# Optimization experiments

Measured on AMD Instinct MI355X. Metric: run time of the kernel, lower is better.

## Reference

```python
import jax, jax.numpy as jnp
import numpy as np

N = 200000   # nodes
R = 4        # relations
E = 1000000  # edges per relation
B = 1024     # graphs in batch


def _graph_conv(h, s, d, ew, W, b):
    """DGL GraphConv, norm='both', optional edge_weight. h:[N,F_in] -> [N,F_out]."""
    n = h.shape[0]
    ones = jnp.ones(s.shape[0], dtype=h.dtype)
    out_deg = jnp.clip(jax.ops.segment_sum(ones, s, num_segments=n), 1.0)
    in_deg = jnp.clip(jax.ops.segment_sum(ones, d, num_segments=n), 1.0)
    hs = h * jax.lax.rsqrt(out_deg)[:, None]          # src-side norm
    m = hs[s]                                         # gather: [E, F_in]
    if ew is not None:
        m = m * ew[:, None]
    agg = jax.ops.segment_sum(m, d, num_segments=n)   # scatter-sum: [N, F_in]
    rst = agg * jax.lax.rsqrt(in_deg)[:, None]        # dst-side norm
    return rst @ W + b


def _hetero_layer(h, src, dst, ew, W, b):
    out = None
    for r in range(R):
        ewr = None if ew is None else ew[r]
        o = _graph_conv(h, src[r], dst[r], ewr, W[r], b[r])
        out = o if out is None else out + o
    return out


def setup_inputs() -> dict:
    key = jax.random.key(0)
    ks = jax.random.split(key, 10)
    feat = jax.random.normal(ks[0], (N, 2), dtype=jnp.float32)
    src = jax.random.randint(ks[1], (R, E), 0, N, dtype=jnp.int32)
    dst = jax.random.randint(ks[2], (R, E), 0, N, dtype=jnp.int32)
    ew = jax.random.uniform(ks[3], (R, E), dtype=jnp.float32)
    graph_ids = jnp.sort(jax.random.randint(ks[4], (N,), 0, B, dtype=jnp.int32))
    W1 = jax.random.normal(ks[5], (R, 2, 16), dtype=jnp.float32) * 0.5
    b1 = jnp.zeros((R, 16), dtype=jnp.float32)
    W2 = jax.random.normal(ks[6], (R, 16, 16), dtype=jnp.float32) * 0.25
    b2 = jnp.zeros((R, 16), dtype=jnp.float32)
    Wc = jax.random.normal(ks[7], (16, 2), dtype=jnp.float32) * 0.25
    bc = jnp.zeros((2,), dtype=jnp.float32)
    return {"feat": feat, "src": src, "dst": dst, "ew": ew,
            "graph_ids": graph_ids, "W1": W1, "b1": b1,
            "W2": W2, "b2": b2, "Wc": Wc, "bc": bc}


def reference(feat, src, dst, ew, graph_ids, W1, b1, W2, b2, Wc, bc):
    # layer 1: per-relation weighted GraphConv, summed over relations
    h = _hetero_layer(feat, src, dst, ew, W1, b1)
    h = jax.nn.relu(h)
    # layer 2: no edge weights (kwargs not forwarded in original code)
    h = _hetero_layer(h, src, dst, None, W2, b2)
    # mean_nodes per graph in the batch
    sums = jax.ops.segment_sum(h, graph_ids, num_segments=B)          # [B,16]
    cnts = jax.ops.segment_sum(jnp.ones((N,), h.dtype), graph_ids, num_segments=B)
    hg = sums / jnp.clip(cnts, 1.0)[:, None]
    return hg @ Wc + bc                                               # [B,2]
```

## Files before the change

### kernel.cpp

```cpp
#include <hip/hip_runtime.h>
#include <hip/hip_fp16.h>

#define NN 200000
#define RR 4
#define EE 1000000
#define BB 1024
#define RN (RR*NN)

#define BSH 7
#define BSZ 128
#define NB 1563
#define RK (RR*NB)
#define EPB 16384
#define SBT 1024
#define BPR ((EE + EPB - 1) / EPB)
#define GSLOTS 32
#define CAPB 1024

#define SRC_OF(u)  (((u) >> 7) & 0x3FFFF)
#define DL_OF(u)   ((int)((u) & 127))
#define DEG_OF(u)  ((u) >> 25)

#define OFF_POOL   0
#define OFF_CNT    (OFF_POOL + BB*16)
#define OFF_GCUR_S (OFF_CNT + BB)
#define OFF_GCUR_D (OFF_GCUR_S + RK)
#define ZERO_UNITS (OFF_GCUR_D + RK)
#define OFF_DEGB   ZERO_UNITS
#define OFF_INVI   (OFF_DEGB + RN/4)
#define OFF_RW16   (OFF_INVI + RN)
#define OFF_AGG1   (OFF_RW16 + RN/2)
#define OFF_H1H    (OFF_AGG1 + RN*2)
#define OFF_KW_    (OFF_H1H + NN*8)
#define OFF_KW     (OFF_KW_ + (OFF_KW_ & 1))


__global__ __launch_bounds__(SBT) void k_scat_src(const int* __restrict__ src,
                                                  int* __restrict__ gcur_s,
                                                  unsigned char* __restrict__ srcbin) {
  __shared__ int cnt[NB];
  __shared__ int base[NB];
  __shared__ int lcur[NB];
  int t = threadIdx.x, r = blockIdx.y, c0 = blockIdx.x * EPB;
  for (int i = t; i < NB; i += SBT) cnt[i] = 0;
  __syncthreads();
  for (int i = t; i < EPB; i += SBT) {
    int e = c0 + i;
    if (e < EE) atomicAdd(&cnt[src[r * EE + e] >> BSH], 1);
  }
  __syncthreads();
  for (int b = t; b < NB; b += SBT) {
    int v = cnt[b];
    base[b] = v ? atomicAdd(&gcur_s[r * NB + b], v) : 0;
    lcur[b] = 0;
  }
  __syncthreads();
  for (int i = t; i < EPB; i += SBT) {
    int e = c0 + i;
    if (e < EE) {
      int s = src[r * EE + e];
      int b = s >> BSH;
      int off = base[b] + atomicAdd(&lcur[b], 1);
      if (off < CAPB)
        srcbin[(size_t)(r * NB + b) * CAPB + off] = (unsigned char)(s & (BSZ - 1));
    }
  }
}

__global__ __launch_bounds__(128) void k_deg(const unsigned char* __restrict__ srcbin,
                                             const int* __restrict__ gcur_s,
                                             unsigned char* __restrict__ degb) {
  __shared__ int cnt[BSZ];
  int t = threadIdx.x, b = blockIdx.x, r = blockIdx.y;
  cnt[t] = 0;
  __syncthreads();
  int k = r * NB + b;
  size_t st = (size_t)k * CAPB;
  int m = min(gcur_s[k], CAPB);
  for (int e = t; e < m; e += 128) atomicAdd(&cnt[srcbin[st + e]], 1);
  __syncthreads();
  int n = (b << BSH) + t;
  if (n < NN) degb[r * NN + n] = (unsigned char)min(max(cnt[t], 1), 63);
}

__global__ __launch_bounds__(SBT) void k_scat_dst(const int* __restrict__ src,
                                                  const int* __restrict__ dst,
                                                  const float* __restrict__ ew,
                                                  const unsigned char* __restrict__ degb,
                                                  int* __restrict__ gcur_d,
                                                  long long* __restrict__ kw) {
  __shared__ int cnt[NB];
  __shared__ int base[NB];
  __shared__ int lcur[NB];
  int t = threadIdx.x, r = blockIdx.y, c0 = blockIdx.x * EPB;
  for (int i = t; i < NB; i += SBT) cnt[i] = 0;
  __syncthreads();
  for (int i = t; i < EPB; i += SBT) {
    int e = c0 + i;
    if (e < EE) atomicAdd(&cnt[dst[r * EE + e] >> BSH], 1);
  }
  __syncthreads();
  for (int b = t; b < NB; b += SBT) {
    int v = cnt[b];
    base[b] = v ? atomicAdd(&gcur_d[r * NB + b], v) : 0;
    lcur[b] = 0;
  }
  __syncthreads();
  for (int i = t; i < EPB; i += SBT) {
    int e = c0 + i;
    if (e < EE) {
      int idx = r * EE + e;
      int d = dst[idx], s = src[idx];
      int b = d >> BSH;
      int off = base[b] + atomicAdd(&lcur[b], 1);
      if (off < CAPB) {
        unsigned dg = degb[r * NN + s];
        float io = rsqrtf((float)dg);
        unsigned short w1h = __half_as_ushort(__float2half_rn(ew[idx] * io));
        unsigned low = (unsigned)(d & (BSZ - 1)) | ((unsigned)s << 7) | (dg << 25);
        kw[(size_t)(r * NB + b) * CAPB + off] =
            (long long)(((unsigned long long)w1h << 32) | low);
      }
    }
  }
}

__global__ __launch_bounds__(256) void k_l1a(long long* __restrict__ kw,
                                             const int* __restrict__ gcur_d,
                                             const float* __restrict__ feat,
                                             float* __restrict__ invi,
                                             unsigned short* __restrict__ rw16,
                                             float* __restrict__ agg1) {
  __shared__ long long bufraw[CAPB];
  __shared__ long long bufsort[CAPB];
  __shared__ int cnt[BSZ];
  __shared__ int scn[BSZ];
  __shared__ int cur[BSZ];
  __shared__ float la[BSZ * 3];
  int t = threadIdx.x, b = blockIdx.x, r = blockIdx.y;
  int n0 = b << BSH;
  int k = r * NB + b;
  size_t st = (size_t)k * CAPB;
  int m = min(gcur_d[k], CAPB);
  if (t < BSZ) { cnt[t] = 0; la[t * 3] = 0.f; la[t * 3 + 1] = 0.f; }
  for (int i = t; i < m; i += 256) bufraw[i] = kw[st + i];
  __syncthreads();
  for (int i = t; i < m; i += 256)
    atomicAdd(&cnt[DL_OF((unsigned)bufraw[i])], 1);
  __syncthreads();
  if (t < BSZ) scn[t] = cnt[t];
  __syncthreads();
  for (int off = 1; off < BSZ; off <<= 1) {
    int v = (t < BSZ && t >= off) ? scn[t - off] : 0;
    __syncthreads();
    if (t < BSZ) scn[t] += v;
    __syncthreads();
  }
  if (t < BSZ) {
    int excl = scn[t] - cnt[t];
    cur[t] = excl;
    int n = n0 + t;
    if (n < NN) {
      invi[r * NN + n] = rsqrtf((float)max(cnt[t], 1));
      rw16[r * NN + n] = (unsigned short)excl;
    }
  }
  __syncthreads();
  for (int i = t; i < m; i += 256) {
    long long kv = bufraw[i];
    bufsort[atomicAdd(&cur[DL_OF((unsigned)kv)], 1)] = kv;
  }
  __syncthreads();
  {
    unsigned* up = (unsigned*)kw + 2 * st + CAPB;
    for (int i = t; i < m; i += 256) up[i] = (unsigned)bufsort[i];
  }
  {
    int f = t & 1, grp = t >> 1;
    int seg = (m + BSZ - 1) >> 7;
    int e = grp * seg;
    int e1 = min(e + seg, m);
    float acc = 0.f;
    int dlprev = -1, dlfirst = -1;
    for (; e < e1; e++) {
      long long kv = bufsort[e];
      unsigned low = (unsigned)kv;
      int dl = DL_OF(low);
      int s = SRC_OF(low);
      float w = __half2float(__ushort_as_half((unsigned short)((unsigned long long)kv >> 32)));
      float fv = feat[s * 2 + f];
      if (dl != dlprev) {
        if (dlprev < 0) dlfirst = dl;
        else if (dlprev == dlfirst) atomicAdd(&la[dlprev * 3 + f], acc);
        else la[dlprev * 3 + f] = acc;
        acc = 0.f; dlprev = dl;
      }
      acc += fv * w;
    }
    if (dlprev >= 0) atomicAdd(&la[dlprev * 3 + f], acc);
  }
  __syncthreads();
  if (t < BSZ) {
    int n = n0 + t;
    if (n < NN)
      ((float2*)agg1)[r * NN + n] = make_float2(la[t * 3], la[t * 3 + 1]);
  }
}

__device__ __forceinline__ unsigned pack2h(float a, float b) {
  __half2 h = __floats2half2_rn(a, b);
  return *reinterpret_cast<unsigned*>(&h);
}

__global__ __launch_bounds__(256) void k_l1b(const float* __restrict__ agg1,
                                             const float* __restrict__ invi,
                                             const float* __restrict__ W1,
                                             const float* __restrict__ b1,
                                             __half* __restrict__ h1h) {
  __shared__ float sW[RR * 2 * 16];
  __shared__ float sb[16];
  int t = threadIdx.x, b = blockIdx.x;
  if (t < RR * 2 * 16) sW[t] = W1[t];
  if (t < 16) {
    float s = 0.f;
    for (int r = 0; r < RR; r++) s += b1[r * 16 + t];
    sb[t] = s;
  }
  __syncthreads();
  int n = b * 256 + t;
  if (n >= NN) return;
  float acc[16];
#pragma unroll
  for (int j = 0; j < 16; j++) acc[j] = sb[j];
#pragma unroll
  for (int r = 0; r < RR; r++) {
    float iv = invi[r * NN + n];
    float2 a = ((const float2*)agg1)[r * NN + n];
    float a0 = a.x * iv, a1 = a.y * iv;
#pragma unroll
    for (int j = 0; j < 16; j++)
      acc[j] += a0 * sW[(r * 2 + 0) * 16 + j] + a1 * sW[(r * 2 + 1) * 16 + j];
  }
#pragma unroll
  for (int j = 0; j < 16; j++) acc[j] = fmaxf(acc[j], 0.f);
  uint4 u0, u1;
  u0.x = pack2h(acc[0], acc[1]);  u0.y = pack2h(acc[2], acc[3]);
  u0.z = pack2h(acc[4], acc[5]);  u0.w = pack2h(acc[6], acc[7]);
  u1.x = pack2h(acc[8], acc[9]);  u1.y = pack2h(acc[10], acc[11]);
  u1.z = pack2h(acc[12], acc[13]); u1.w = pack2h(acc[14], acc[15]);
  uint4* o = (uint4*)(h1h + (size_t)n * 16);
  o[0] = u0; o[1] = u1;
}

__device__ __forceinline__ void acc8(float* acc, uint4 u, float w) {
  float2 p;
  p = __half22float2(*(__half2*)&u.x); acc[0] += p.x * w; acc[1] += p.y * w;
  p = __half22float2(*(__half2*)&u.y); acc[2] += p.x * w; acc[3] += p.y * w;
  p = __half22float2(*(__half2*)&u.z); acc[4] += p.x * w; acc[5] += p.y * w;
  p = __half22float2(*(__half2*)&u.w); acc[6] += p.x * w; acc[7] += p.y * w;
}

__global__ __launch_bounds__(256) void k_l2(const long long* __restrict__ kw,
                                            const int* __restrict__ gcur_d,
                                            const unsigned short* __restrict__ rw16,
                                            const __half* __restrict__ h1h,
                                            const float* __restrict__ invi,
                                            const float* __restrict__ W2,
                                            const int* __restrict__ gid,
                                            float* __restrict__ pool,
                                            float* __restrict__ cnt) {
  __shared__ float agg[BSZ * 17];
  __shared__ float sW[16 * 16];
  __shared__ int   sg[BSZ];
  __shared__ unsigned short srw[BSZ + 1];
  __shared__ float gslot[GSLOTS * 16];
  __shared__ int   cslot[GSLOTS];
  __shared__ int   present[GSLOTS];
  int t = threadIdx.x, b = blockIdx.x, r = blockIdx.y;
  int n0 = b << BSH;
  int k = r * NB + b;
  int m = min(gcur_d[k], CAPB);
  sW[t] = W2[r * 256 + t];
  if (t < GSLOTS) { cslot[t] = 0; present[t] = 0; }
  for (int i = t; i < GSLOTS * 16; i += 256) gslot[i] = 0.f;
  if (t < BSZ) {
    int n = n0 + t;
    srw[t] = (n < NN) ? rw16[r * NN + n] : (unsigned short)m;
  }
  if (t == BSZ) srw[BSZ] = (unsigned short)m;
  __syncthreads();
  const uint4* h4p = (const uint4*)h1h;
  const unsigned* rb = (const unsigned*)kw + 2 * (size_t)k * CAPB + CAPB;
  int f8 = t & 1, g = t >> 1;
  int e = srw[g], en = srw[g + 1];
  float acc[8];
#pragma unroll
  for (int j = 0; j < 8; j++) acc[j] = 0.f;
  for (; e + 3 < en; e += 4) {
    unsigned r0 = rb[e], r1 = rb[e + 1], r2 = rb[e + 2], r3 = rb[e + 3];
    uint4 u0 = h4p[(size_t)SRC_OF(r0) * 2 + f8];
    uint4 u1 = h4p[(size_t)SRC_OF(r1) * 2 + f8];
    uint4 u2 = h4p[(size_t)SRC_OF(r2) * 2 + f8];
    uint4 u3 = h4p[(size_t)SRC_OF(r3) * 2 + f8];
    acc8(acc, u0, rsqrtf((float)DEG_OF(r0)));
    acc8(acc, u1, rsqrtf((float)DEG_OF(r1)));
    acc8(acc, u2, rsqrtf((float)DEG_OF(r2)));
    acc8(acc, u3, rsqrtf((float)DEG_OF(r3)));
  }
  for (; e < en; e++) {
    unsigned rr = rb[e];
    uint4 u = h4p[(size_t)SRC_OF(rr) * 2 + f8];
    acc8(acc, u, rsqrtf((float)DEG_OF(rr)));
  }
#pragma unroll
  for (int j = 0; j < 8; j++) agg[g * 17 + 8 * f8 + j] = acc[j];
  __syncthreads();
  int n = n0 + t;
  int g0 = gid[n0];
  bool valid = (t < BSZ) && (n < NN);
  float out[16];
#pragma unroll
  for (int j = 0; j < 16; j++) out[j] = 0.f;
  if (valid) {
    float iv = invi[r * NN + n];
#pragma unroll
    for (int kk = 0; kk < 16; kk++) {
      float a = agg[t * 17 + kk] * iv;
#pragma unroll
      for (int j = 0; j < 16; j++) out[j] += a * sW[kk * 16 + j];
    }
  }
  __syncthreads();
  if (t < BSZ) {
    sg[t] = valid ? (gid[n] - g0) : -1;
#pragma unroll
    for (int j = 0; j < 16; j++) agg[t * 17 + j] = out[j];
  }
  __syncthreads();
  {
    int f = t & 15, i0 = t >> 4;
    for (int i = i0; i < BSZ; i += 16) {
      int gsN = sg[i];
      if (gsN < 0) continue;
      float v = agg[i * 17 + f];
      if (gsN < GSLOTS) {
        atomicAdd(&gslot[gsN * 16 + f], v);
        if (f == 0) {
          present[gsN] = 1;
          if (r == 0) atomicAdd(&cslot[gsN], 1);
        }
      } else {
        atomicAdd(&pool[(g0 + gsN) * 16 + f], v);
        if (f == 0 && r == 0) atomicAdd(&cnt[g0 + gsN], 1.0f);
      }
    }
  }
  __syncthreads();
  if (t < GSLOTS * 16) {
    int gsN = t >> 4, f = t & 15;
    if (present[gsN]) atomicAdd(&pool[(g0 + gsN) * 16 + f], gslot[t]);
  }
  if (r == 0 && t < GSLOTS && cslot[t] > 0)
    atomicAdd(&cnt[g0 + t], (float)cslot[t]);
}

__global__ __launch_bounds__(256) void k_final(const float* __restrict__ pool,
                                               const float* __restrict__ cnt,
                                               const float* __restrict__ b2,
                                               const float* __restrict__ Wc,
                                               const float* __restrict__ bc,
                                               float* __restrict__ out) {
  int b = blockIdx.x * 256 + threadIdx.x;
  if (b >= BB) return;
  float c = cnt[b];
  float inv = 1.0f / fmaxf(c, 1.0f);
  float o0 = bc[0], o1 = bc[1];
#pragma unroll
  for (int j = 0; j < 16; j++) {
    float sb = 0.f;
    for (int r = 0; r < RR; r++) sb += b2[r * 16 + j];
    float v = (pool[b * 16 + j] + c * sb) * inv;
    o0 += v * Wc[j * 2 + 0];
    o1 += v * Wc[j * 2 + 1];
  }
  out[b * 2 + 0] = o0;
  out[b * 2 + 1] = o1;
}

extern "C" void kernel_launch(void* const* d_in, const int* in_sizes, int n_in,
                              void* d_out, int out_size, void* d_ws, size_t ws_size,
                              hipStream_t stream) {
  const float* feat = (const float*)d_in[0];
  const int*   src  = (const int*)d_in[1];
  const int*   dst  = (const int*)d_in[2];
  const float* ew   = (const float*)d_in[3];
  const int*   gid  = (const int*)d_in[4];
  const float* W1   = (const float*)d_in[5];
  const float* b1   = (const float*)d_in[6];
  const float* W2   = (const float*)d_in[7];
  const float* b2   = (const float*)d_in[8];
  const float* Wc   = (const float*)d_in[9];
  const float* bc   = (const float*)d_in[10];

  char* ws = (char*)d_ws;
  float* pool   = (float*)(ws + (size_t)OFF_POOL   * 4);
  float* cnt    = (float*)(ws + (size_t)OFF_CNT    * 4);
  int*   gcur_s = (int*)  (ws + (size_t)OFF_GCUR_S * 4);
  int*   gcur_d = (int*)  (ws + (size_t)OFF_GCUR_D * 4);
  unsigned char*  degb = (unsigned char*) (ws + (size_t)OFF_DEGB * 4);
  float* invi   = (float*)(ws + (size_t)OFF_INVI   * 4);
  unsigned short* rw16 = (unsigned short*)(ws + (size_t)OFF_RW16 * 4);
  float* agg1   = (float*)(ws + (size_t)OFF_AGG1   * 4);
  __half* h1h   = (__half*)(ws + (size_t)OFF_H1H   * 4);
  long long* kw = (long long*)(ws + (size_t)OFF_KW * 4);

  hipMemsetAsync(d_ws, 0, (size_t)ZERO_UNITS * 4, stream);

  k_scat_src<<<dim3(BPR, RR), SBT, 0, stream>>>(src, gcur_s, (unsigned char*)kw);
  k_deg     <<<dim3(NB, RR), 128, 0, stream>>>((const unsigned char*)kw, gcur_s, degb);
  k_scat_dst<<<dim3(BPR, RR), SBT, 0, stream>>>(src, dst, ew, degb, gcur_d, kw);
  k_l1a     <<<dim3(NB, RR), 256, 0, stream>>>(kw, gcur_d, feat, invi, rw16, agg1);
  k_l1b     <<<(NN + 255) / 256, 256, 0, stream>>>(agg1, invi, W1, b1, h1h);
  k_l2      <<<dim3(NB, RR), 256, 0, stream>>>(kw, gcur_d, rw16, h1h, invi, W2, gid, pool, cnt);
  k_final   <<<(BB + 255) / 256, 256, 0, stream>>>(pool, cnt, b2, Wc, bc, (float*)d_out);
}
```

Measured before the change: 342.5 us.

## Replace two-pass source binning with direct global atomic degree counting

Out-degree is now counted with global atomicAdd on a per-relation int32 array, using vectorized int4 loads of src, instead of binning sources into buckets and then histogramming each bucket. This removes one scatter kernel and one histogram kernel, along with the byte-sized bin writes. In exchange it needs an extra memset of an int32 degree array that aliases the h1h region, and it pays for random global atomics. The edges-per-block value for the dst scatter is also halved to launch more blocks.

```diff
diff --git a/kernel.cpp b/kernel.cpp
--- a/kernel.cpp
+++ b/kernel.cpp
@@ -11,9 +11,10 @@
 #define BSZ 128
 #define NB 1563
 #define RK (RR*NB)
-#define EPB 16384
+#define EPB 8192
 #define SBT 1024
 #define BPR ((EE + EPB - 1) / EPB)
+#define DGB ((EE/4 + 255) / 256)
 #define GSLOTS 32
 #define CAPB 1024
 
@@ -23,70 +24,34 @@
 
 #define OFF_POOL   0
 #define OFF_CNT    (OFF_POOL + BB*16)
-#define OFF_GCUR_S (OFF_CNT + BB)
-#define OFF_GCUR_D (OFF_GCUR_S + RK)
+#define OFF_GCUR_D (OFF_CNT + BB)
 #define ZERO_UNITS (OFF_GCUR_D + RK)
-#define OFF_DEGB   ZERO_UNITS
-#define OFF_INVI   (OFF_DEGB + RN/4)
+#define OFF_INVI   ZERO_UNITS
 #define OFF_RW16   (OFF_INVI + RN)
 #define OFF_AGG1   (OFF_RW16 + RN/2)
 #define OFF_H1H    (OFF_AGG1 + RN*2)
+#define OFF_DEG32  OFF_H1H
 #define OFF_KW_    (OFF_H1H + NN*8)
 #define OFF_KW     (OFF_KW_ + (OFF_KW_ & 1))
 
 
-__global__ __launch_bounds__(SBT) void k_scat_src(const int* __restrict__ src,
-                                                  int* __restrict__ gcur_s,
-                                                  unsigned char* __restrict__ srcbin) {
-  __shared__ int cnt[NB];
-  __shared__ int base[NB];
-  __shared__ int lcur[NB];
-  int t = threadIdx.x, r = blockIdx.y, c0 = blockIdx.x * EPB;
-  for (int i = t; i < NB; i += SBT) cnt[i] = 0;
-  __syncthreads();
-  for (int i = t; i < EPB; i += SBT) {
-    int e = c0 + i;
-    if (e < EE) atomicAdd(&cnt[src[r * EE + e] >> BSH], 1);
-  }
-  __syncthreads();
-  for (int b = t; b < NB; b += SBT) {
-    int v = cnt[b];
-    base[b] = v ? atomicAdd(&gcur_s[r * NB + b], v) : 0;
-    lcur[b] = 0;
-  }
-  __syncthreads();
-  for (int i = t; i < EPB; i += SBT) {
-    int e = c0 + i;
-    if (e < EE) {
-      int s = src[r * EE + e];
-      int b = s >> BSH;
-      int off = base[b] + atomicAdd(&lcur[b], 1);
-      if (off < CAPB)
-        srcbin[(size_t)(r * NB + b) * CAPB + off] = (unsigned char)(s & (BSZ - 1));
-    }
-  }
-}
-
-__global__ __launch_bounds__(128) void k_deg(const unsigned char* __restrict__ srcbin,
-                                             const int* __restrict__ gcur_s,
-                                             unsigned char* __restrict__ degb) {
-  __shared__ int cnt[BSZ];
-  int t = threadIdx.x, b = blockIdx.x, r = blockIdx.y;
-  cnt[t] = 0;
-  __syncthreads();
-  int k = r * NB + b;
-  size_t st = (size_t)k * CAPB;
-  int m = min(gcur_s[k], CAPB);
-  for (int e = t; e < m; e += 128) atomicAdd(&cnt[srcbin[st + e]], 1);
-  __syncthreads();
-  int n = (b << BSH) + t;
-  if (n < NN) degb[r * NN + n] = (unsigned char)min(max(cnt[t], 1), 63);
+__global__ __launch_bounds__(256) void k_degcnt(const int* __restrict__ src,
+                                                int* __restrict__ deg32) {
+  int r = blockIdx.y;
+  int i = blockIdx.x * 256 + threadIdx.x;
+  if (i >= EE / 4) return;
+  int4 s4 = ((const int4*)(src + (size_t)r * EE))[i];
+  int* d = deg32 + r * NN;
+  atomicAdd(&d[s4.x], 1);
+  atomicAdd(&d[s4.y], 1);
+  atomicAdd(&d[s4.z], 1);
+  atomicAdd(&d[s4.w], 1);
 }
 
 __global__ __launch_bounds__(SBT) void k_scat_dst(const int* __restrict__ src,
                                                   const int* __restrict__ dst,
                                                   const float* __restrict__ ew,
-                                                  const unsigned char* __restrict__ degb,
+                                                  const int* __restrict__ deg32,
                                                   int* __restrict__ gcur_d,
                                                   long long* __restrict__ kw) {
   __shared__ int cnt[NB];
@@ -114,7 +79,7 @@
       int b = d >> BSH;
       int off = base[b] + atomicAdd(&lcur[b], 1);
       if (off < CAPB) {
-        unsigned dg = degb[r * NN + s];
+        unsigned dg = (unsigned)min(max(deg32[r * NN + s], 1), 63);
         float io = rsqrtf((float)dg);
         unsigned short w1h = __half_as_ushort(__float2half_rn(ew[idx] * io));
         unsigned low = (unsigned)(d & (BSZ - 1)) | ((unsigned)s << 7) | (dg << 25);
@@ -405,20 +370,19 @@
   char* ws = (char*)d_ws;
   float* pool   = (float*)(ws + (size_t)OFF_POOL   * 4);
   float* cnt    = (float*)(ws + (size_t)OFF_CNT    * 4);
-  int*   gcur_s = (int*)  (ws + (size_t)OFF_GCUR_S * 4);
   int*   gcur_d = (int*)  (ws + (size_t)OFF_GCUR_D * 4);
-  unsigned char*  degb = (unsigned char*) (ws + (size_t)OFF_DEGB * 4);
   float* invi   = (float*)(ws + (size_t)OFF_INVI   * 4);
   unsigned short* rw16 = (unsigned short*)(ws + (size_t)OFF_RW16 * 4);
   float* agg1   = (float*)(ws + (size_t)OFF_AGG1   * 4);
   __half* h1h   = (__half*)(ws + (size_t)OFF_H1H   * 4);
+  int*   deg32  = (int*)  (ws + (size_t)OFF_DEG32  * 4);
   long long* kw = (long long*)(ws + (size_t)OFF_KW * 4);
 
   hipMemsetAsync(d_ws, 0, (size_t)ZERO_UNITS * 4, stream);
-
-  k_scat_src<<<dim3(BPR, RR), SBT, 0, stream>>>(src, gcur_s, (unsigned char*)kw);
-  k_deg     <<<dim3(NB, RR), 128, 0, stream>>>((const unsigned char*)kw, gcur_s, degb);
-  k_scat_dst<<<dim3(BPR, RR), SBT, 0, stream>>>(src, dst, ew, degb, gcur_d, kw);
+  hipMemsetAsync(ws + (size_t)OFF_DEG32 * 4, 0, (size_t)RN * 4, stream);
+
+  k_degcnt  <<<dim3(DGB, RR), 256, 0, stream>>>(src, deg32);
+  k_scat_dst<<<dim3(BPR, RR), SBT, 0, stream>>>(src, dst, ew, deg32, gcur_d, kw);
   k_l1a     <<<dim3(NB, RR), 256, 0, stream>>>(kw, gcur_d, feat, invi, rw16, agg1);
   k_l1b     <<<(NN + 255) / 256, 256, 0, stream>>>(agg1, invi, W1, b1, h1h);
   k_l2      <<<dim3(NB, RR), 256, 0, stream>>>(kw, gcur_d, rw16, h1h, invi, W2, gid, pool, cnt);
```

After: 468.6 us. +36.8%, slower.
